# Kernel optimization log

Hardware: AMD Instinct MI355X
Metric: run time of the kernel (lower is better)

The kernel has to match this reference:

```python
import jax, jax.numpy as jnp
import numpy as np

EPS = 1e-6
ROPE_BASE = 10000.0


def rmsnorm(x, w):
    return x * jax.lax.rsqrt(jnp.mean(x * x, axis=-1, keepdims=True) + EPS) * w


def apply_rope(x, start_pos):
    # x: [B, H, S, Dh]
    B, H, S, Dh = x.shape
    inv_freq = 1.0 / (ROPE_BASE ** (jnp.arange(0, Dh, 2, dtype=jnp.float32) / Dh))
    pos = jnp.arange(S, dtype=jnp.float32) + start_pos
    ang = pos[:, None] * inv_freq[None, :]            # [S, Dh/2]
    cos, sin = jnp.cos(ang), jnp.sin(ang)
    x1, x2 = jnp.split(x, 2, axis=-1)
    return jnp.concatenate([x1 * cos - x2 * sin, x1 * sin + x2 * cos], axis=-1)


def block_forward(x, norm1_w, norm2_w, wq, w_dkv, w_uk, w_uv, wo, gate_w, w1, w2, w3, start_pos, n_head, d_head, top_k):
    B, S, D = x.shape
    E = w1.shape[0]

    # ---- MLA attention (pre-norm) ----
    h = rmsnorm(x, norm1_w)
    q = (h @ wq).reshape(B, S, n_head, d_head).transpose(0, 2, 1, 3)   # [B,H,S,Dh]
    c = h @ w_dkv                                                      # [B,S,d_latent]
    k = (c @ w_uk).reshape(B, S, n_head, d_head).transpose(0, 2, 1, 3)
    v = (c @ w_uv).reshape(B, S, n_head, d_head).transpose(0, 2, 1, 3)
    q = apply_rope(q, start_pos)
    k = apply_rope(k, start_pos)
    scores = jnp.einsum('bhqd,bhkd->bhqk', q, k) / jnp.sqrt(jnp.float32(d_head))
    causal = jnp.tril(jnp.ones((S, S), dtype=bool))
    scores = jnp.where(causal, scores, jnp.finfo(scores.dtype).min)
    attn = jax.nn.softmax(scores, axis=-1)
    a = jnp.einsum('bhqk,bhkd->bhqd', attn, v).transpose(0, 2, 1, 3).reshape(B, S, n_head * d_head)
    x = x + a @ wo

    # ---- MoE FFN (pre-norm) ----
    h2 = rmsnorm(x, norm2_w)
    xf = h2.reshape(B * S, D)                                          # [T,D]
    logits = xf @ gate_w                                               # [T,E]
    probs = jax.nn.softmax(logits, axis=-1)
    topv, topi = jax.lax.top_k(probs, top_k)                           # [T,k]
    topv = topv / jnp.sum(topv, axis=-1, keepdims=True)
    one_hot = jax.nn.one_hot(topi, E, dtype=probs.dtype)               # [T,k,E]
    combine = jnp.einsum('tk,tke->te', topv, one_hot)                  # [T,E]

    y = jnp.zeros_like(xf)
    for e in range(E):  # fixed small expert count; masked dense combine (no token drop)
        g = jax.nn.silu(xf @ w1[e]) * (xf @ w3[e])
        y = y + combine[:, e:e + 1] * (g @ w2[e])

    # load-balancing aux loss: E * sum(frac_routed * mean_prob)
    f = jnp.mean(one_hot, axis=(0, 1)) * top_k
    P = jnp.mean(probs, axis=0)
    aux_loss = jnp.float32(E) * jnp.sum(f * P)

    x = x + y.reshape(B, S, D)
    return x, aux_loss


def setup_inputs() -> dict:
    key = jax.random.key(0)
    D, H, Dh, DL, E, HID = 768, 12, 64, 64, 8, 4 * 768
    B, S = 2, 512
    ks = jax.random.split(key, 12)
    s = 0.02
    return {
        'x': jax.random.normal(ks[0], (B, S, D), jnp.float32),
        'norm1_w': jnp.ones((D,), jnp.float32),
        'norm2_w': jnp.ones((D,), jnp.float32),
        'wq': jax.random.normal(ks[1], (D, H * Dh), jnp.float32) * s,
        'w_dkv': jax.random.normal(ks[2], (D, DL), jnp.float32) * s,
        'w_uk': jax.random.normal(ks[3], (DL, H * Dh), jnp.float32) * s,
        'w_uv': jax.random.normal(ks[4], (DL, H * Dh), jnp.float32) * s,
        'wo': jax.random.normal(ks[5], (H * Dh, D), jnp.float32) * s,
        'gate_w': jax.random.normal(ks[6], (D, E), jnp.float32) * s,
        'w1': jax.random.normal(ks[7], (E, D, HID), jnp.float32) * s,
        'w2': jax.random.normal(ks[8], (E, HID, D), jnp.float32) * s,
        'w3': jax.random.normal(ks[9], (E, D, HID), jnp.float32) * s,
        'start_pos': 0,
    }


def reference(x, norm1_w, norm2_w, wq, w_dkv, w_uk, w_uv, wo, gate_w, w1, w2, w3, start_pos):
    return block_forward(x, norm1_w, norm2_w, wq, w_dkv, w_uk, w_uv, wo, gate_w, w1, w2, w3,
                         start_pos, n_head=12, d_head=64, top_k=2)
```

## Files before the change

kernel.cpp:

```cpp
#include <hip/hip_runtime.h>
#include <hip/hip_bf16.h>
#include <math.h>

#define T 1024
#define SEQ 512
#define BATCH 2
#define D 768
#define H 12
#define DH 64
#define DL 64
#define E 8
#define HID 3072

typedef __attribute__((ext_vector_type(8))) short bf16x8;
typedef __attribute__((ext_vector_type(4))) float f32x4;

__device__ inline short f2bf(float f) {
    __hip_bfloat16 h = __float2bfloat16(f);
    return *reinterpret_cast<short*>(&h);
}

__device__ inline void lds_barrier() {
    __builtin_amdgcn_sched_barrier(0);
    asm volatile("s_waitcnt lgkmcnt(0)" ::: "memory");
    __builtin_amdgcn_s_barrier();
    __builtin_amdgcn_sched_barrier(0);
}

__device__ inline int swz(int row, int k) { return (row * 64 + k) ^ ((row & 7) << 3); }
__device__ inline int swzB(int row, int k) { return row * 64 + (k ^ (((row >> 1) & 7) << 3)); }

__global__ void rmsnorm_kernel(const float* __restrict__ x, const float* __restrict__ w,
                               float* __restrict__ out, short* __restrict__ outb) {
    int t = blockIdx.x;
    int tid = threadIdx.x;
    const float* xr = x + (size_t)t * D;
    float s = 0.f;
    for (int i = tid; i < D; i += 256) { float v = xr[i]; s += v * v; }
    __shared__ float red[256];
    red[tid] = s; __syncthreads();
    for (int o = 128; o > 0; o >>= 1) { if (tid < o) red[tid] += red[tid + o]; __syncthreads(); }
    float scale = 1.0f / sqrtf(red[0] / (float)D + 1e-6f);
    for (int i = tid; i < D; i += 256) {
        float v = xr[i] * scale * w[i];
        out[(size_t)t * D + i] = v;
        outb[(size_t)t * D + i] = f2bf(v);
    }
}

template<bool RES>
__global__ __launch_bounds__(256) void gemm_bf16(
    const float* __restrict__ A, const float* __restrict__ B,
    const float* __restrict__ Rp, float* __restrict__ C,
    int M, int N, int K) {
    int mb = blockIdx.y * 64, nb = blockIdx.x * 64;
    __shared__ short As[64 * 64];
    __shared__ short Bs[64 * 64];
    int tid = threadIdx.x;
    int lane = tid & 63, wave = tid >> 6;
    int wr = wave >> 1, wc = wave & 1;
    f32x4 acc[2][2] = {};
    int ar = tid >> 2, ac = (tid & 3) * 16;
    int bn = (tid & 15) * 4, bk = (tid >> 4) * 4;
    const float* Arow = A + (size_t)(mb + ar) * K + ac;
    const float* Bg = B + nb;
    float4 a_r[4], b_r[4];
#pragma unroll
    for (int j = 0; j < 4; j++) a_r[j] = *(const float4*)(Arow + j * 4);
#pragma unroll
    for (int i = 0; i < 4; i++) b_r[i] = *(const float4*)(Bg + (size_t)(bk + i) * N + bn);
    for (int k0 = 0; k0 < K; k0 += 64) {
#pragma unroll
        for (int j = 0; j < 4; j++)
            *(short4*)&As[swzB(ar, ac + j * 4)] =
                make_short4(f2bf(a_r[j].x), f2bf(a_r[j].y), f2bf(a_r[j].z), f2bf(a_r[j].w));
        *(short4*)&Bs[swzB(bn + 0, bk)] = make_short4(f2bf(b_r[0].x), f2bf(b_r[1].x), f2bf(b_r[2].x), f2bf(b_r[3].x));
        *(short4*)&Bs[swzB(bn + 1, bk)] = make_short4(f2bf(b_r[0].y), f2bf(b_r[1].y), f2bf(b_r[2].y), f2bf(b_r[3].y));
        *(short4*)&Bs[swzB(bn + 2, bk)] = make_short4(f2bf(b_r[0].z), f2bf(b_r[1].z), f2bf(b_r[2].z), f2bf(b_r[3].z));
        *(short4*)&Bs[swzB(bn + 3, bk)] = make_short4(f2bf(b_r[0].w), f2bf(b_r[1].w), f2bf(b_r[2].w), f2bf(b_r[3].w));
        __syncthreads();
        bool more = (k0 + 64) < K;
        if (more) {
#pragma unroll
            for (int j = 0; j < 4; j++) a_r[j] = *(const float4*)(Arow + k0 + 64 + j * 4);
#pragma unroll
            for (int i = 0; i < 4; i++) b_r[i] = *(const float4*)(Bg + (size_t)(k0 + 64 + bk + i) * N + bn);
        }
#pragma unroll
        for (int kk = 0; kk < 64; kk += 32) {
            int krd = kk + 8 * (lane >> 4);
            bf16x8 a0 = *(const bf16x8*)&As[swzB(wr * 32 + (lane & 15), krd)];
            bf16x8 a1 = *(const bf16x8*)&As[swzB(wr * 32 + 16 + (lane & 15), krd)];
            bf16x8 b0 = *(const bf16x8*)&Bs[swzB(wc * 32 + (lane & 15), krd)];
            bf16x8 b1 = *(const bf16x8*)&Bs[swzB(wc * 32 + 16 + (lane & 15), krd)];
            acc[0][0] = __builtin_amdgcn_mfma_f32_16x16x32_bf16(a0, b0, acc[0][0], 0, 0, 0);
            acc[0][1] = __builtin_amdgcn_mfma_f32_16x16x32_bf16(a0, b1, acc[0][1], 0, 0, 0);
            acc[1][0] = __builtin_amdgcn_mfma_f32_16x16x32_bf16(a1, b0, acc[1][0], 0, 0, 0);
            acc[1][1] = __builtin_amdgcn_mfma_f32_16x16x32_bf16(a1, b1, acc[1][1], 0, 0, 0);
        }
        __syncthreads();
    }
#pragma unroll
    for (int mi = 0; mi < 2; mi++)
#pragma unroll
        for (int ni = 0; ni < 2; ni++)
#pragma unroll
            for (int r = 0; r < 4; r++) {
                int row = mb + wr * 32 + mi * 16 + (lane >> 4) * 4 + r;
                int col = nb + wc * 32 + ni * 16 + (lane & 15);
                float val = acc[mi][ni][r];
                if (RES) val += Rp[(size_t)row * N + col];
                C[(size_t)row * N + col] = val;
            }
}

__global__ __launch_bounds__(256) void gemm_qdkv(
    const float* __restrict__ A, const float* __restrict__ Bq, const float* __restrict__ Bd,
    float* __restrict__ Cq, float* __restrict__ Cd) {
    int bx = blockIdx.x;
    const float* Bsel; float* Csel; int N; int nb;
    if (bx < D / 64) { Bsel = Bq; Csel = Cq; N = D;  nb = bx * 64; }
    else             { Bsel = Bd; Csel = Cd; N = DL; nb = 0; }
    int mb = blockIdx.y * 64;
    __shared__ short As[64 * 64];
    __shared__ short Bs[64 * 64];
    int tid = threadIdx.x;
    int lane = tid & 63, wave = tid >> 6;
    int wr = wave >> 1, wc = wave & 1;
    f32x4 acc[2][2] = {};
    int ar = tid >> 2, ac = (tid & 3) * 16;
    int bn = (tid & 15) * 4, bk = (tid >> 4) * 4;
    const float* Arow = A + (size_t)(mb + ar) * D + ac;
    const float* Bg = Bsel + nb;
    float4 a_r[4], b_r[4];
#pragma unroll
    for (int j = 0; j < 4; j++) a_r[j] = *(const float4*)(Arow + j * 4);
#pragma unroll
    for (int i = 0; i < 4; i++) b_r[i] = *(const float4*)(Bg + (size_t)(bk + i) * N + bn);
    for (int k0 = 0; k0 < D; k0 += 64) {
#pragma unroll
        for (int j = 0; j < 4; j++)
            *(short4*)&As[swzB(ar, ac + j * 4)] =
                make_short4(f2bf(a_r[j].x), f2bf(a_r[j].y), f2bf(a_r[j].z), f2bf(a_r[j].w));
        *(short4*)&Bs[swzB(bn + 0, bk)] = make_short4(f2bf(b_r[0].x), f2bf(b_r[1].x), f2bf(b_r[2].x), f2bf(b_r[3].x));
        *(short4*)&Bs[swzB(bn + 1, bk)] = make_short4(f2bf(b_r[0].y), f2bf(b_r[1].y), f2bf(b_r[2].y), f2bf(b_r[3].y));
        *(short4*)&Bs[swzB(bn + 2, bk)] = make_short4(f2bf(b_r[0].z), f2bf(b_r[1].z), f2bf(b_r[2].z), f2bf(b_r[3].z));
        *(short4*)&Bs[swzB(bn + 3, bk)] = make_short4(f2bf(b_r[0].w), f2bf(b_r[1].w), f2bf(b_r[2].w), f2bf(b_r[3].w));
        __syncthreads();
        bool more = (k0 + 64) < D;
        if (more) {
#pragma unroll
            for (int j = 0; j < 4; j++) a_r[j] = *(const float4*)(Arow + k0 + 64 + j * 4);
#pragma unroll
            for (int i = 0; i < 4; i++) b_r[i] = *(const float4*)(Bg + (size_t)(k0 + 64 + bk + i) * N + bn);
        }
#pragma unroll
        for (int kk = 0; kk < 64; kk += 32) {
            int krd = kk + 8 * (lane >> 4);
            bf16x8 a0 = *(const bf16x8*)&As[swzB(wr * 32 + (lane & 15), krd)];
            bf16x8 a1 = *(const bf16x8*)&As[swzB(wr * 32 + 16 + (lane & 15), krd)];
            bf16x8 b0 = *(const bf16x8*)&Bs[swzB(wc * 32 + (lane & 15), krd)];
            bf16x8 b1 = *(const bf16x8*)&Bs[swzB(wc * 32 + 16 + (lane & 15), krd)];
            acc[0][0] = __builtin_amdgcn_mfma_f32_16x16x32_bf16(a0, b0, acc[0][0], 0, 0, 0);
            acc[0][1] = __builtin_amdgcn_mfma_f32_16x16x32_bf16(a0, b1, acc[0][1], 0, 0, 0);
            acc[1][0] = __builtin_amdgcn_mfma_f32_16x16x32_bf16(a1, b0, acc[1][0], 0, 0, 0);
            acc[1][1] = __builtin_amdgcn_mfma_f32_16x16x32_bf16(a1, b1, acc[1][1], 0, 0, 0);
        }
        __syncthreads();
    }
#pragma unroll
    for (int mi = 0; mi < 2; mi++)
#pragma unroll
        for (int ni = 0; ni < 2; ni++)
#pragma unroll
            for (int r = 0; r < 4; r++) {
                int row = mb + wr * 32 + mi * 16 + (lane >> 4) * 4 + r;
                int col = nb + wc * 32 + ni * 16 + (lane & 15);
                Csel[(size_t)row * N + col] = acc[mi][ni][r];
            }
}

__global__ __launch_bounds__(256) void gemm_kuv(
    const float* __restrict__ A, const float* __restrict__ Bk, const float* __restrict__ Bv,
    float* __restrict__ Ck, float* __restrict__ Cv, int M, int N, int K) {
    int mb = blockIdx.y * 64, nb = blockIdx.x * 64;
    __shared__ short As[64 * 64];
    __shared__ short B1s[64 * 64];
    __shared__ short B2s[64 * 64];
    int tid = threadIdx.x;
    int lane = tid & 63, wave = tid >> 6;
    int wr = wave >> 1, wc = wave & 1;
    f32x4 acc1[2][2] = {};
    f32x4 acc2[2][2] = {};
    int ar = tid >> 2, ac = (tid & 3) * 16;
    int bn = (tid & 15) * 4, bk = (tid >> 4) * 4;
    const float* Arow = A + (size_t)(mb + ar) * K + ac;
    {
        float4 a_c[4], p_c[4], q_c[4];
#pragma unroll
        for (int j = 0; j < 4; j++) a_c[j] = *(const float4*)(Arow + j * 4);
#pragma unroll
        for (int i = 0; i < 4; i++) {
            p_c[i] = *(const float4*)(Bk + (size_t)(bk + i) * N + nb + bn);
            q_c[i] = *(const float4*)(Bv + (size_t)(bk + i) * N + nb + bn);
        }
#pragma unroll
        for (int j = 0; j < 4; j++)
            *(short4*)&As[swzB(ar, ac + j * 4)] =
                make_short4(f2bf(a_c[j].x), f2bf(a_c[j].y), f2bf(a_c[j].z), f2bf(a_c[j].w));
        *(short4*)&B1s[swzB(bn + 0, bk)] = make_short4(f2bf(p_c[0].x), f2bf(p_c[1].x), f2bf(p_c[2].x), f2bf(p_c[3].x));
        *(short4*)&B1s[swzB(bn + 1, bk)] = make_short4(f2bf(p_c[0].y), f2bf(p_c[1].y), f2bf(p_c[2].y), f2bf(p_c[3].y));
        *(short4*)&B1s[swzB(bn + 2, bk)] = make_short4(f2bf(p_c[0].z), f2bf(p_c[1].z), f2bf(p_c[2].z), f2bf(p_c[3].z));
        *(short4*)&B1s[swzB(bn + 3, bk)] = make_short4(f2bf(p_c[0].w), f2bf(p_c[1].w), f2bf(p_c[2].w), f2bf(p_c[3].w));
        *(short4*)&B2s[swzB(bn + 0, bk)] = make_short4(f2bf(q_c[0].x), f2bf(q_c[1].x), f2bf(q_c[2].x), f2bf(q_c[3].x));
        *(short4*)&B2s[swzB(bn + 1, bk)] = make_short4(f2bf(q_c[0].y), f2bf(q_c[1].y), f2bf(q_c[2].y), f2bf(q_c[3].y));
        *(short4*)&B2s[swzB(bn + 2, bk)] = make_short4(f2bf(q_c[0].z), f2bf(q_c[1].z), f2bf(q_c[2].z), f2bf(q_c[3].z));
        *(short4*)&B2s[swzB(bn + 3, bk)] = make_short4(f2bf(q_c[0].w), f2bf(q_c[1].w), f2bf(q_c[2].w), f2bf(q_c[3].w));
    }
    __syncthreads();
#pragma unroll
    for (int kk = 0; kk < 64; kk += 32) {
        int krd = kk + 8 * (lane >> 4);
        bf16x8 a0 = *(const bf16x8*)&As[swzB(wr * 32 + (lane & 15), krd)];
        bf16x8 a1 = *(const bf16x8*)&As[swzB(wr * 32 + 16 + (lane & 15), krd)];
        bf16x8 p0 = *(const bf16x8*)&B1s[swzB(wc * 32 + (lane & 15), krd)];
        bf16x8 p1 = *(const bf16x8*)&B1s[swzB(wc * 32 + 16 + (lane & 15), krd)];
        bf16x8 q0 = *(const bf16x8*)&B2s[swzB(wc * 32 + (lane & 15), krd)];
        bf16x8 q1 = *(const bf16x8*)&B2s[swzB(wc * 32 + 16 + (lane & 15), krd)];
        acc1[0][0] = __builtin_amdgcn_mfma_f32_16x16x32_bf16(a0, p0, acc1[0][0], 0, 0, 0);
        acc1[0][1] = __builtin_amdgcn_mfma_f32_16x16x32_bf16(a0, p1, acc1[0][1], 0, 0, 0);
        acc1[1][0] = __builtin_amdgcn_mfma_f32_16x16x32_bf16(a1, p0, acc1[1][0], 0, 0, 0);
        acc1[1][1] = __builtin_amdgcn_mfma_f32_16x16x32_bf16(a1, p1, acc1[1][1], 0, 0, 0);
        acc2[0][0] = __builtin_amdgcn_mfma_f32_16x16x32_bf16(a0, q0, acc2[0][0], 0, 0, 0);
        acc2[0][1] = __builtin_amdgcn_mfma_f32_16x16x32_bf16(a0, q1, acc2[0][1], 0, 0, 0);
        acc2[1][0] = __builtin_amdgcn_mfma_f32_16x16x32_bf16(a1, q0, acc2[1][0], 0, 0, 0);
        acc2[1][1] = __builtin_amdgcn_mfma_f32_16x16x32_bf16(a1, q1, acc2[1][1], 0, 0, 0);
    }
#pragma unroll
    for (int mi = 0; mi < 2; mi++)
#pragma unroll
        for (int ni = 0; ni < 2; ni++)
#pragma unroll
            for (int r = 0; r < 4; r++) {
                int row = mb + wr * 32 + mi * 16 + (lane >> 4) * 4 + r;
                int col = nb + wc * 32 + ni * 16 + (lane & 15);
                Ck[(size_t)row * N + col] = acc1[mi][ni][r];
                Cv[(size_t)row * N + col] = acc2[mi][ni][r];
            }
}

__global__ void rope_kernel(float* __restrict__ qb, float* __restrict__ kb,
                            const int* __restrict__ spp) {
    int p = blockIdx.x * 256 + threadIdx.x;
    if (p >= T * H * 32) return;
    int i = p & 31;
    int rem = p >> 5;
    int h = rem % H;
    int ts = rem / H;
    int s = ts % SEQ;
    float invf = powf(10000.0f, -(float)(2 * i) / 64.0f);
    float ang = (float)(s + spp[0]) * invf;
    float c = cosf(ang), sn = sinf(ang);
    size_t base = (size_t)ts * D + h * DH;
    float x1 = qb[base + i], x2 = qb[base + 32 + i];
    qb[base + i] = x1 * c - x2 * sn;
    qb[base + 32 + i] = x1 * sn + x2 * c;
    x1 = kb[base + i]; x2 = kb[base + 32 + i];
    kb[base + i] = x1 * c - x2 * sn;
    kb[base + 32 + i] = x1 * sn + x2 * c;
}

__global__ __launch_bounds__(256) void attn_mfma(
    const float* __restrict__ q, const float* __restrict__ k,
    const float* __restrict__ v, float* __restrict__ a) {
    int qt = blockIdx.x, h = blockIdx.y, b = blockIdx.z;
    int tid = threadIdx.x, lane = tid & 63, wave = tid >> 6;
    __shared__ short Qs[64 * 64];
    __shared__ short Ks[64 * 64];
    __shared__ short Vs[64 * 64];
    __shared__ short Ps[64 * 64];
    int qbase = qt * 64;
    {
        int r = tid >> 2, d0 = (tid & 3) * 16;
        const float* src = q + ((size_t)(b * SEQ + qbase + r)) * D + h * DH + d0;
#pragma unroll
        for (int j = 0; j < 4; j++) {
            float4 vv = *(const float4*)(src + j * 4);
            *(short4*)&Qs[swz(r, d0 + j * 4)] =
                make_short4(f2bf(vv.x), f2bf(vv.y), f2bf(vv.z), f2bf(vv.w));
        }
    }
    __syncthreads();
    bf16x8 qf0 = *(const bf16x8*)&Qs[swz(wave * 16 + (lane & 15), 8 * (lane >> 4))];
    bf16x8 qf1 = *(const bf16x8*)&Qs[swz(wave * 16 + (lane & 15), 32 + 8 * (lane >> 4))];

    float m_run[4] = {-1e30f, -1e30f, -1e30f, -1e30f};
    float l_run[4] = {0.f, 0.f, 0.f, 0.f};
    f32x4 o[4] = {};

    for (int kt = 0; kt <= qt; kt++) {
        int kvbase = kt * 64;
        {
            int r = tid >> 2, d0 = (tid & 3) * 16;
            const float* src = k + ((size_t)(b * SEQ + kvbase + r)) * D + h * DH + d0;
#pragma unroll
            for (int j = 0; j < 4; j++) {
                float4 vv = *(const float4*)(src + j * 4);
                *(short4*)&Ks[swz(r, d0 + j * 4)] =
                    make_short4(f2bf(vv.x), f2bf(vv.y), f2bf(vv.z), f2bf(vv.w));
            }
        }
#pragma unroll
        for (int i = 0; i < 4; i++) {
            int idx = tid + i * 256;
            int kr = idx >> 4, d0 = (idx & 15) * 4;
            float4 vv = *(const float4*)(v + ((size_t)(b * SEQ + kvbase + kr)) * D + h * DH + d0);
            Vs[swz(d0 + 0, kr)] = f2bf(vv.x); Vs[swz(d0 + 1, kr)] = f2bf(vv.y);
            Vs[swz(d0 + 2, kr)] = f2bf(vv.z); Vs[swz(d0 + 3, kr)] = f2bf(vv.w);
        }
        __syncthreads();

        f32x4 s[4];
#pragma unroll
        for (int kvt = 0; kvt < 4; kvt++) {
            bf16x8 kf0 = *(const bf16x8*)&Ks[swz(kvt * 16 + (lane & 15), 8 * (lane >> 4))];
            bf16x8 kf1 = *(const bf16x8*)&Ks[swz(kvt * 16 + (lane & 15), 32 + 8 * (lane >> 4))];
            f32x4 z = {};
            z = __builtin_amdgcn_mfma_f32_16x16x32_bf16(qf0, kf0, z, 0, 0, 0);
            z = __builtin_amdgcn_mfma_f32_16x16x32_bf16(qf1, kf1, z, 0, 0, 0);
            s[kvt] = z;
        }
#pragma unroll
        for (int kvt = 0; kvt < 4; kvt++) {
#pragma unroll
            for (int r = 0; r < 4; r++) {
                float val = s[kvt][r] * 0.125f;
                if (kt == qt) {
                    int kv_abs = kvbase + kvt * 16 + (lane & 15);
                    int q_abs = qbase + wave * 16 + (lane >> 4) * 4 + r;
                    if (kv_abs > q_abs) val = -1e30f;
                }
                s[kvt][r] = val;
            }
        }
        float mnew[4], psum[4], scl[4];
#pragma unroll
        for (int r = 0; r < 4; r++) {
            float mx = fmaxf(fmaxf(s[0][r], s[1][r]), fmaxf(s[2][r], s[3][r]));
#pragma unroll
            for (int o2 = 8; o2 > 0; o2 >>= 1) mx = fmaxf(mx, __shfl_xor(mx, o2));
            mnew[r] = fmaxf(m_run[r], mx);
            float ps = 0.f;
#pragma unroll
            for (int kvt = 0; kvt < 4; kvt++) {
                float p = expf(s[kvt][r] - mnew[r]);
                s[kvt][r] = p;
                ps += p;
            }
#pragma unroll
            for (int o2 = 8; o2 > 0; o2 >>= 1) ps += __shfl_xor(ps, o2);
            psum[r] = ps;
            scl[r] = expf(m_run[r] - mnew[r]);
            m_run[r] = mnew[r];
            l_run[r] = l_run[r] * scl[r] + psum[r];
        }
#pragma unroll
        for (int dt = 0; dt < 4; dt++)
#pragma unroll
            for (int r = 0; r < 4; r++) o[dt][r] *= scl[r];
#pragma unroll
        for (int kvt = 0; kvt < 4; kvt++)
#pragma unroll
            for (int r = 0; r < 4; r++)
                Ps[swz(wave * 16 + (lane >> 4) * 4 + r, kvt * 16 + (lane & 15))] = f2bf(s[kvt][r]);
        __syncthreads();
        bf16x8 pa0 = *(const bf16x8*)&Ps[swz(wave * 16 + (lane & 15), 8 * (lane >> 4))];
        bf16x8 pa1 = *(const bf16x8*)&Ps[swz(wave * 16 + (lane & 15), 32 + 8 * (lane >> 4))];
#pragma unroll
        for (int dt = 0; dt < 4; dt++) {
            bf16x8 vf0 = *(const bf16x8*)&Vs[swz(dt * 16 + (lane & 15), 8 * (lane >> 4))];
            bf16x8 vf1 = *(const bf16x8*)&Vs[swz(dt * 16 + (lane & 15), 32 + 8 * (lane >> 4))];
            o[dt] = __builtin_amdgcn_mfma_f32_16x16x32_bf16(pa0, vf0, o[dt], 0, 0, 0);
            o[dt] = __builtin_amdgcn_mfma_f32_16x16x32_bf16(pa1, vf1, o[dt], 0, 0, 0);
        }
        __syncthreads();
    }
#pragma unroll
    for (int r = 0; r < 4; r++) {
        float inv = 1.0f / l_run[r];
        int qrow = qbase + wave * 16 + (lane >> 4) * 4 + r;
#pragma unroll
        for (int dt = 0; dt < 4; dt++) {
            a[((size_t)(b * SEQ + qrow)) * D + h * DH + dt * 16 + (lane & 15)] = o[dt][r] * inv;
        }
    }
}

__global__ void routing_kernel(const float* __restrict__ h2, const float* __restrict__ gw,
                               float* __restrict__ probs, int* __restrict__ list,
                               int* __restrict__ counts, float* __restrict__ wtok) {
    int t = blockIdx.x;
    int tid = threadIdx.x;
    __shared__ float part[64][8];
    float l[8] = {0.f, 0.f, 0.f, 0.f, 0.f, 0.f, 0.f, 0.f};
    const float* hr = h2 + (size_t)t * D;
    for (int i = tid; i < D; i += 64) {
        float hv = hr[i];
        const float* g = gw + (size_t)i * E;
#pragma unroll
        for (int e = 0; e < 8; e++) l[e] += hv * g[e];
    }
#pragma unroll
    for (int e = 0; e < 8; e++) part[tid][e] = l[e];
    __syncthreads();
    if (tid == 0) {
        float lg[8];
#pragma unroll
        for (int e = 0; e < 8; e++) {
            float s = 0.f;
            for (int j = 0; j < 64; j++) s += part[j][e];
            lg[e] = s;
        }
        float m = lg[0];
#pragma unroll
        for (int e = 1; e < 8; e++) m = fmaxf(m, lg[e]);
        float se = 0.f;
        float pr[8];
#pragma unroll
        for (int e = 0; e < 8; e++) { pr[e] = expf(lg[e] - m); se += pr[e]; }
#pragma unroll
        for (int e = 0; e < 8; e++) { pr[e] /= se; probs[t * 8 + e] = pr[e]; }
        int i0 = 0;
#pragma unroll
        for (int e = 1; e < 8; e++) if (pr[e] > pr[i0]) i0 = e;
        int i1 = -1;
#pragma unroll
        for (int e = 0; e < 8; e++) {
            if (e == i0) continue;
            if (i1 < 0 || pr[e] > pr[i1]) i1 = e;
        }
        float w0 = pr[i0], w1 = pr[i1];
        float wsum = w0 + w1;
        wtok[t * 2 + 0] = w0 / wsum;
        wtok[t * 2 + 1] = w1 / wsum;
        int p0 = atomicAdd(&counts[i0], 1); list[i0 * T + p0] = t * 2 + 0;
        int p1 = atomicAdd(&counts[i1], 1); list[i1 * T + p1] = t * 2 + 1;
    }
}

__global__ void moe_setup_kernel(const int* __restrict__ counts,
                                 int* __restrict__ m2e_u, int* __restrict__ m2mb_u,
                                 int* __restrict__ m2e_d, int* __restrict__ m2mb_d,
                                 int* __restrict__ ntm) {
    if (threadIdx.x == 0 && blockIdx.x == 0) {
        int idx = 0;
        for (int e = 0; e < E; e++) {
            int nt = (counts[e] + 127) >> 7;
            for (int i = 0; i < nt; i++) { m2e_u[idx] = e; m2mb_u[idx] = i * 128; idx++; }
        }
        ntm[0] = idx;
        idx = 0;
        for (int e = 0; e < E; e++) {
            int nt = (counts[e] + 63) >> 6;
            for (int i = 0; i < nt; i++) { m2e_d[idx] = e; m2mb_d[idx] = i * 64; idx++; }
        }
        ntm[1] = idx;
    }
}

__global__ void aux_kernel(const float* __restrict__ probs, const int* __restrict__ counts,
                           float* __restrict__ out_aux) {
    int tid = threadIdx.x;
    float part[8] = {0.f, 0.f, 0.f, 0.f, 0.f, 0.f, 0.f, 0.f};
    for (int t = tid; t < T; t += 256) {
#pragma unroll
        for (int e = 0; e < 8; e++) part[e] += probs[t * 8 + e];
    }
    __shared__ float red[256][8];
#pragma unroll
    for (int e = 0; e < 8; e++) red[tid][e] = part[e];
    __syncthreads();
    for (int o = 128; o > 0; o >>= 1) {
        if (tid < o) {
#pragma unroll
            for (int e = 0; e < 8; e++) red[tid][e] += red[tid + o][e];
        }
        __syncthreads();
    }
    if (tid == 0) {
        float aux = 0.f;
        for (int e = 0; e < 8; e++) {
            float f = (float)counts[e] / (float)T;
            float P = red[0][e] / (float)T;
            aux += f * P;
        }
        out_aux[0] = (float)E * aux;
    }
}

__global__ __launch_bounds__(256) void moe_up_mfma(
    const short* __restrict__ h2b, const float* __restrict__ w1, const float* __restrict__ w3,
    const int* __restrict__ list, const int* __restrict__ counts,
    const int* __restrict__ m2e, const int* __restrict__ m2mb, const int* __restrict__ ntm,
    short* __restrict__ g) {
    int mi = blockIdx.y;
    if (mi >= ntm[0]) return;
    int e = m2e[mi];
    int mb = m2mb[mi];
    int n = counts[e];
    int nb = blockIdx.x * 64;
    const float* B1g = w1 + (size_t)e * D * HID + nb;
    const float* B3g = w3 + (size_t)e * D * HID + nb;
    __shared__ short As[2][128 * 64];
    __shared__ short B1s[2][64 * 64];
    __shared__ short B3s[2][64 * 64];
    __shared__ int rowpid[128];
    __shared__ int rowtok[128];
    int tid = threadIdx.x;
    int lane = tid & 63, wave = tid >> 6;
    int wr = wave >> 1, wc = wave & 1;
    if (tid < 128) {
        int r = mb + tid;
        int pid = (r < n) ? list[e * T + r] : list[e * T];
        rowpid[tid] = pid;
        rowtok[tid] = pid >> 1;
    }
    __syncthreads();

    f32x4 acc1[4][2] = {};
    f32x4 acc3[4][2] = {};
    int ar = tid >> 1, ac = (tid & 1) * 32;
    int bn = (tid & 15) * 4, bk = (tid >> 4) * 4;
    const short* Arow = h2b + (size_t)rowtok[ar] * D + ac;

    bf16x8 a_r[4];
    float4 b1_r[4], b3_r[4];
#pragma unroll
    for (int j = 0; j < 4; j++) a_r[j] = *(const bf16x8*)(Arow + j * 8);
#pragma unroll
    for (int i = 0; i < 4; i++) {
        b1_r[i] = *(const float4*)(B1g + (size_t)(bk + i) * HID + bn);
        b3_r[i] = *(const float4*)(B3g + (size_t)(bk + i) * HID + bn);
    }
#pragma unroll
    for (int j = 0; j < 4; j++) *(bf16x8*)&As[0][swzB(ar, ac + j * 8)] = a_r[j];
    *(short4*)&B1s[0][swzB(bn + 0, bk)] = make_short4(f2bf(b1_r[0].x), f2bf(b1_r[1].x), f2bf(b1_r[2].x), f2bf(b1_r[3].x));
    *(short4*)&B1s[0][swzB(bn + 1, bk)] = make_short4(f2bf(b1_r[0].y), f2bf(b1_r[1].y), f2bf(b1_r[2].y), f2bf(b1_r[3].y));
    *(short4*)&B1s[0][swzB(bn + 2, bk)] = make_short4(f2bf(b1_r[0].z), f2bf(b1_r[1].z), f2bf(b1_r[2].z), f2bf(b1_r[3].z));
    *(short4*)&B1s[0][swzB(bn + 3, bk)] = make_short4(f2bf(b1_r[0].w), f2bf(b1_r[1].w), f2bf(b1_r[2].w), f2bf(b1_r[3].w));
    *(short4*)&B3s[0][swzB(bn + 0, bk)] = make_short4(f2bf(b3_r[0].x), f2bf(b3_r[1].x), f2bf(b3_r[2].x), f2bf(b3_r[3].x));
    *(short4*)&B3s[0][swzB(bn + 1, bk)] = make_short4(f2bf(b3_r[0].y), f2bf(b3_r[1].y), f2bf(b3_r[2].y), f2bf(b3_r[3].y));
    *(short4*)&B3s[0][swzB(bn + 2, bk)] = make_short4(f2bf(b3_r[0].z), f2bf(b3_r[1].z), f2bf(b3_r[2].z), f2bf(b3_r[3].z));
    *(short4*)&B3s[0][swzB(bn + 3, bk)] = make_short4(f2bf(b3_r[0].w), f2bf(b3_r[1].w), f2bf(b3_r[2].w), f2bf(b3_r[3].w));
    lds_barrier();
#pragma unroll
    for (int j = 0; j < 4; j++) a_r[j] = *(const bf16x8*)(Arow + 64 + j * 8);
#pragma unroll
    for (int i = 0; i < 4; i++) {
        b1_r[i] = *(const float4*)(B1g + (size_t)(64 + bk + i) * HID + bn);
        b3_r[i] = *(const float4*)(B3g + (size_t)(64 + bk + i) * HID + bn);
    }

    int cur = 0;
    for (int k0 = 0; k0 < D; k0 += 64) {
        bool more = (k0 + 64) < D;
        if (more) {
            int nx = cur ^ 1;
#pragma unroll
            for (int j = 0; j < 4; j++) *(bf16x8*)&As[nx][swzB(ar, ac + j * 8)] = a_r[j];
            *(short4*)&B1s[nx][swzB(bn + 0, bk)] = make_short4(f2bf(b1_r[0].x), f2bf(b1_r[1].x), f2bf(b1_r[2].x), f2bf(b1_r[3].x));
            *(short4*)&B1s[nx][swzB(bn + 1, bk)] = make_short4(f2bf(b1_r[0].y), f2bf(b1_r[1].y), f2bf(b1_r[2].y), f2bf(b1_r[3].y));
            *(short4*)&B1s[nx][swzB(bn + 2, bk)] = make_short4(f2bf(b1_r[0].z), f2bf(b1_r[1].z), f2bf(b1_r[2].z), f2bf(b1_r[3].z));
            *(short4*)&B1s[nx][swzB(bn + 3, bk)] = make_short4(f2bf(b1_r[0].w), f2bf(b1_r[1].w), f2bf(b1_r[2].w), f2bf(b1_r[3].w));
            *(short4*)&B3s[nx][swzB(bn + 0, bk)] = make_short4(f2bf(b3_r[0].x), f2bf(b3_r[1].x), f2bf(b3_r[2].x), f2bf(b3_r[3].x));
            *(short4*)&B3s[nx][swzB(bn + 1, bk)] = make_short4(f2bf(b3_r[0].y), f2bf(b3_r[1].y), f2bf(b3_r[2].y), f2bf(b3_r[3].y));
            *(short4*)&B3s[nx][swzB(bn + 2, bk)] = make_short4(f2bf(b3_r[0].z), f2bf(b3_r[1].z), f2bf(b3_r[2].z), f2bf(b3_r[3].z));
            *(short4*)&B3s[nx][swzB(bn + 3, bk)] = make_short4(f2bf(b3_r[0].w), f2bf(b3_r[1].w), f2bf(b3_r[2].w), f2bf(b3_r[3].w));
        }
        if (k0 + 128 < D) {
#pragma unroll
            for (int j = 0; j < 4; j++) a_r[j] = *(const bf16x8*)(Arow + k0 + 128 + j * 8);
#pragma unroll
            for (int i = 0; i < 4; i++) {
                b1_r[i] = *(const float4*)(B1g + (size_t)(k0 + 128 + bk + i) * HID + bn);
                b3_r[i] = *(const float4*)(B3g + (size_t)(k0 + 128 + bk + i) * HID + bn);
            }
        }
#pragma unroll
        for (int kk = 0; kk < 64; kk += 32) {
            int krd = kk + 8 * (lane >> 4);
            bf16x8 b1f[2], b3f[2];
#pragma unroll
            for (int ni = 0; ni < 2; ni++) {
                b1f[ni] = *(const bf16x8*)&B1s[cur][swzB(wc * 32 + ni * 16 + (lane & 15), krd)];
                b3f[ni] = *(const bf16x8*)&B3s[cur][swzB(wc * 32 + ni * 16 + (lane & 15), krd)];
            }
#pragma unroll
            for (int mi2 = 0; mi2 < 4; mi2++) {
                bf16x8 af = *(const bf16x8*)&As[cur][swzB(wr * 64 + mi2 * 16 + (lane & 15), krd)];
                acc1[mi2][0] = __builtin_amdgcn_mfma_f32_16x16x32_bf16(af, b1f[0], acc1[mi2][0], 0, 0, 0);
                acc1[mi2][1] = __builtin_amdgcn_mfma_f32_16x16x32_bf16(af, b1f[1], acc1[mi2][1], 0, 0, 0);
                acc3[mi2][0] = __builtin_amdgcn_mfma_f32_16x16x32_bf16(af, b3f[0], acc3[mi2][0], 0, 0, 0);
                acc3[mi2][1] = __builtin_amdgcn_mfma_f32_16x16x32_bf16(af, b3f[1], acc3[mi2][1], 0, 0, 0);
            }
        }
        lds_barrier();
        cur ^= 1;
    }
#pragma unroll
    for (int mi2 = 0; mi2 < 4; mi2++)
#pragma unroll
        for (int ni = 0; ni < 2; ni++)
#pragma unroll
            for (int r = 0; r < 4; r++) {
                int row = wr * 64 + mi2 * 16 + (lane >> 4) * 4 + r;
                if (mb + row < n) {
                    int pid = rowpid[row];
                    int col = nb + wc * 32 + ni * 16 + (lane & 15);
                    float v1 = acc1[mi2][ni][r], v3 = acc3[mi2][ni][r];
                    float sil = v1 / (1.f + expf(-v1));
                    g[(size_t)pid * HID + col] = f2bf(sil * v3);
                }
            }
}

__global__ __launch_bounds__(256) void moe_down_mfma(
    const short* __restrict__ g, const float* __restrict__ w2,
    const int* __restrict__ list, const int* __restrict__ counts,
    const int* __restrict__ m2e, const int* __restrict__ m2mb, const int* __restrict__ ntm,
    float* __restrict__ yp) {
    int mi = blockIdx.y;
    if (mi >= ntm[1]) return;
    int e = m2e[mi];
    int mb = m2mb[mi];
    int n = counts[e];
    int nb = blockIdx.x * 64;
    const float* Bg = w2 + (size_t)e * HID * D + nb;
    __shared__ short As[64 * 64];
    __shared__ short Bs[64 * 64];
    __shared__ int rowpid[64];
    int tid = threadIdx.x;
    int lane = tid & 63, wave = tid >> 6;
    int wr = wave >> 1, wc = wave & 1;
    if (tid < 64) {
        int r = mb + tid;
        rowpid[tid] = (r < n) ? list[e * T + r] : list[e * T];
    }
    __syncthreads();

    f32x4 acc[2][2] = {};
    int ar0 = tid >> 3, ak0 = (tid & 7) * 8;
    int ar1 = (tid + 256) >> 3, ak1 = ((tid + 256) & 7) * 8;
    int bn = (tid & 15) * 4, bk = (tid >> 4) * 4;
    const short* Asrc0 = g + (size_t)rowpid[ar0] * HID + ak0;
    const short* Asrc1 = g + (size_t)rowpid[ar1] * HID + ak1;

    bf16x8 a_r0 = *(const bf16x8*)(Asrc0);
    bf16x8 a_r1 = *(const bf16x8*)(Asrc1);
    float4 b_r[4];
#pragma unroll
    for (int i = 0; i < 4; i++) b_r[i] = *(const float4*)(Bg + (size_t)(bk + i) * D + bn);

    for (int k0 = 0; k0 < HID; k0 += 64) {
        *(bf16x8*)&As[swzB(ar0, ak0)] = a_r0;
        *(bf16x8*)&As[swzB(ar1, ak1)] = a_r1;
        *(short4*)&Bs[swzB(bn + 0, bk)] = make_short4(f2bf(b_r[0].x), f2bf(b_r[1].x), f2bf(b_r[2].x), f2bf(b_r[3].x));
        *(short4*)&Bs[swzB(bn + 1, bk)] = make_short4(f2bf(b_r[0].y), f2bf(b_r[1].y), f2bf(b_r[2].y), f2bf(b_r[3].y));
        *(short4*)&Bs[swzB(bn + 2, bk)] = make_short4(f2bf(b_r[0].z), f2bf(b_r[1].z), f2bf(b_r[2].z), f2bf(b_r[3].z));
        *(short4*)&Bs[swzB(bn + 3, bk)] = make_short4(f2bf(b_r[0].w), f2bf(b_r[1].w), f2bf(b_r[2].w), f2bf(b_r[3].w));
        lds_barrier();
        bool more = (k0 + 64) < HID;
        if (more) {
            a_r0 = *(const bf16x8*)(Asrc0 + k0 + 64);
            a_r1 = *(const bf16x8*)(Asrc1 + k0 + 64);
#pragma unroll
            for (int i = 0; i < 4; i++) b_r[i] = *(const float4*)(Bg + (size_t)(k0 + 64 + bk + i) * D + bn);
        }
#pragma unroll
        for (int kk = 0; kk < 64; kk += 32) {
            int krd = kk + 8 * (lane >> 4);
            bf16x8 a0 = *(const bf16x8*)&As[swzB(wr * 32 + (lane & 15), krd)];
            bf16x8 a1 = *(const bf16x8*)&As[swzB(wr * 32 + 16 + (lane & 15), krd)];
            bf16x8 b0 = *(const bf16x8*)&Bs[swzB(wc * 32 + (lane & 15), krd)];
            bf16x8 b1 = *(const bf16x8*)&Bs[swzB(wc * 32 + 16 + (lane & 15), krd)];
            acc[0][0] = __builtin_amdgcn_mfma_f32_16x16x32_bf16(a0, b0, acc[0][0], 0, 0, 0);
            acc[0][1] = __builtin_amdgcn_mfma_f32_16x16x32_bf16(a0, b1, acc[0][1], 0, 0, 0);
            acc[1][0] = __builtin_amdgcn_mfma_f32_16x16x32_bf16(a1, b0, acc[1][0], 0, 0, 0);
            acc[1][1] = __builtin_amdgcn_mfma_f32_16x16x32_bf16(a1, b1, acc[1][1], 0, 0, 0);
        }
        lds_barrier();
    }
#pragma unroll
    for (int mi2 = 0; mi2 < 2; mi2++)
#pragma unroll
        for (int ni = 0; ni < 2; ni++)
#pragma unroll
            for (int r = 0; r < 4; r++) {
                int row = wr * 32 + mi2 * 16 + (lane >> 4) * 4 + r;
                if (mb + row < n) {
                    int pid = rowpid[row];
                    int col = nb + wc * 32 + ni * 16 + (lane & 15);
                    yp[(size_t)pid * D + col] = acc[mi2][ni][r];
                }
            }
}

__global__ void combine_kernel(const float* __restrict__ yp, const float* __restrict__ wtok,
                               float* __restrict__ out) {
    int idx = blockIdx.x * 256 + threadIdx.x;
    if (idx >= T * (D / 4)) return;
    int t = idx / (D / 4);
    int d4 = idx % (D / 4);
    float4 a = ((const float4*)(out + (size_t)t * D))[d4];
    float4 y0 = ((const float4*)(yp + (size_t)(2 * t) * D))[d4];
    float4 y1 = ((const float4*)(yp + (size_t)(2 * t + 1) * D))[d4];
    float w0 = wtok[2 * t], w1 = wtok[2 * t + 1];
    a.x += w0 * y0.x + w1 * y1.x;
    a.y += w0 * y0.y + w1 * y1.y;
    a.z += w0 * y0.z + w1 * y1.z;
    a.w += w0 * y0.w + w1 * y1.w;
    ((float4*)(out + (size_t)t * D))[d4] = a;
}

extern "C" void kernel_launch(void* const* d_in, const int* in_sizes, int n_in,
                              void* d_out, int out_size, void* d_ws, size_t ws_size,
                              hipStream_t stream) {
    const float* x    = (const float*)d_in[0];
    const float* n1w  = (const float*)d_in[1];
    const float* n2w  = (const float*)d_in[2];
    const float* wq   = (const float*)d_in[3];
    const float* wdkv = (const float*)d_in[4];
    const float* wuk  = (const float*)d_in[5];
    const float* wuv  = (const float*)d_in[6];
    const float* wo   = (const float*)d_in[7];
    const float* gw   = (const float*)d_in[8];
    const float* w1   = (const float*)d_in[9];
    const float* w2   = (const float*)d_in[10];
    const float* w3   = (const float*)d_in[11];
    const int*   sp   = (const int*)d_in[12];
    float* out = (float*)d_out;

    float* ws = (float*)d_ws;
    float* A_  = ws + 0;
    float* B_  = ws + 786432;
    float* C_  = ws + 1572864;
    float* Dd  = ws + 2359296;
    float* cb  = ws + 3145728;
    float* probs = ws + 3211264;
    float* wtok  = ws + 3219456;
    int*   list  = (int*)(ws + 3221504);
    int*   counts= (int*)(ws + 3229696);
    int*   m2e_u = (int*)(ws + 3229712);
    int*   m2mb_u= (int*)(ws + 3229744);
    int*   m2e_d = (int*)(ws + 3229776);
    int*   m2mb_d= (int*)(ws + 3229840);
    int*   ntm   = (int*)(ws + 3229904);
    short* h2b   = (short*)(ws + 3229920);
    short* gch   = (short*)(ws + 3623136);
    float* yp = B_;

    hipMemsetAsync(counts, 0, 16 * sizeof(int), stream);

    rmsnorm_kernel<<<T, 256, 0, stream>>>(x, n1w, Dd, h2b);
    gemm_qdkv<<<dim3(D / 64 + 1, T / 64), 256, 0, stream>>>(Dd, wq, wdkv, A_, cb);
    gemm_kuv<<<dim3(D / 64, T / 64), 256, 0, stream>>>(cb, wuk, wuv, B_, C_, T, D, DL);
    rope_kernel<<<(T * H * 32 + 255) / 256, 256, 0, stream>>>(A_, B_, sp);
    attn_mfma<<<dim3(8, H, BATCH), 256, 0, stream>>>(A_, B_, C_, Dd);
    gemm_bf16<true><<<dim3(D / 64, T / 64), 256, 0, stream>>>(Dd, wo, x, out, T, D, D);

    rmsnorm_kernel<<<T, 256, 0, stream>>>(out, n2w, A_, h2b);
    routing_kernel<<<T, 64, 0, stream>>>(A_, gw, probs, list, counts, wtok);
    moe_setup_kernel<<<1, 64, 0, stream>>>(counts, m2e_u, m2mb_u, m2e_d, m2mb_d, ntm);
    aux_kernel<<<1, 256, 0, stream>>>(probs, counts, out + (out_size - 1));
    moe_up_mfma<<<dim3(HID / 64, 32), 256, 0, stream>>>(h2b, w1, w3, list, counts, m2e_u, m2mb_u, ntm, gch);
    moe_down_mfma<<<dim3(D / 64, 40), 256, 0, stream>>>(gch, w2, list, counts, m2e_d, m2mb_d, ntm, yp);
    combine_kernel<<<(T * (D / 4) + 255) / 256, 256, 0, stream>>>(yp, wtok, out);
}
```

Baseline: 219.9 us.

## Enlarge MoE down-proj M tile to 128 and double-buffer LDS

The MoE down-projection kernel now processes 128 token rows per block instead of 64, reusing the up-projection's 128-row tile mapping (m2e_u/m2mb_u, ntm[0]). It also double-buffers the A and B LDS tiles, so each iteration needs only one barrier and the global loads run two steps ahead. The larger tile halves the number of w2 tile reads and raises MFMA work per B fragment. In exchange LDS use and register pressure grow, and fewer blocks are launched, which can lower occupancy.

```diff
diff --git a/kernel.cpp b/kernel.cpp
--- a/kernel.cpp
+++ b/kernel.cpp
@@ -630,73 +630,89 @@
     const int* __restrict__ m2e, const int* __restrict__ m2mb, const int* __restrict__ ntm,
     float* __restrict__ yp) {
     int mi = blockIdx.y;
-    if (mi >= ntm[1]) return;
+    if (mi >= ntm[0]) return;
     int e = m2e[mi];
     int mb = m2mb[mi];
     int n = counts[e];
     int nb = blockIdx.x * 64;
     const float* Bg = w2 + (size_t)e * HID * D + nb;
-    __shared__ short As[64 * 64];
-    __shared__ short Bs[64 * 64];
-    __shared__ int rowpid[64];
+    __shared__ short As[2][128 * 64];
+    __shared__ short Bs[2][64 * 64];
+    __shared__ int rowpid[128];
     int tid = threadIdx.x;
     int lane = tid & 63, wave = tid >> 6;
     int wr = wave >> 1, wc = wave & 1;
-    if (tid < 64) {
+    if (tid < 128) {
         int r = mb + tid;
         rowpid[tid] = (r < n) ? list[e * T + r] : list[e * T];
     }
     __syncthreads();
 
-    f32x4 acc[2][2] = {};
-    int ar0 = tid >> 3, ak0 = (tid & 7) * 8;
-    int ar1 = (tid + 256) >> 3, ak1 = ((tid + 256) & 7) * 8;
+    f32x4 acc[4][2] = {};
+    int ar = tid >> 1, ac = (tid & 1) * 32;
     int bn = (tid & 15) * 4, bk = (tid >> 4) * 4;
-    const short* Asrc0 = g + (size_t)rowpid[ar0] * HID + ak0;
-    const short* Asrc1 = g + (size_t)rowpid[ar1] * HID + ak1;
-
-    bf16x8 a_r0 = *(const bf16x8*)(Asrc0);
-    bf16x8 a_r1 = *(const bf16x8*)(Asrc1);
+    const short* Arow = g + (size_t)rowpid[ar] * HID + ac;
+
+    bf16x8 a_r[4];
     float4 b_r[4];
 #pragma unroll
+    for (int j = 0; j < 4; j++) a_r[j] = *(const bf16x8*)(Arow + j * 8);
+#pragma unroll
     for (int i = 0; i < 4; i++) b_r[i] = *(const float4*)(Bg + (size_t)(bk + i) * D + bn);
-
+#pragma unroll
+    for (int j = 0; j < 4; j++) *(bf16x8*)&As[0][swzB(ar, ac + j * 8)] = a_r[j];
+    *(short4*)&Bs[0][swzB(bn + 0, bk)] = make_short4(f2bf(b_r[0].x), f2bf(b_r[1].x), f2bf(b_r[2].x), f2bf(b_r[3].x));
+    *(short4*)&Bs[0][swzB(bn + 1, bk)] = make_short4(f2bf(b_r[0].y), f2bf(b_r[1].y), f2bf(b_r[2].y), f2bf(b_r[3].y));
+    *(short4*)&Bs[0][swzB(bn + 2, bk)] = make_short4(f2bf(b_r[0].z), f2bf(b_r[1].z), f2bf(b_r[2].z), f2bf(b_r[3].z));
+    *(short4*)&Bs[0][swzB(bn + 3, bk)] = make_short4(f2bf(b_r[0].w), f2bf(b_r[1].w), f2bf(b_r[2].w), f2bf(b_r[3].w));
+    lds_barrier();
+#pragma unroll
+    for (int j = 0; j < 4; j++) a_r[j] = *(const bf16x8*)(Arow + 64 + j * 8);
+#pragma unroll
+    for (int i = 0; i < 4; i++) b_r[i] = *(const float4*)(Bg + (size_t)(64 + bk + i) * D + bn);
+
+    int cur = 0;
     for (int k0 = 0; k0 < HID; k0 += 64) {
-        *(bf16x8*)&As[swzB(ar0, ak0)] = a_r0;
-        *(bf16x8*)&As[swzB(ar1, ak1)] = a_r1;
-        *(short4*)&Bs[swzB(bn + 0, bk)] = make_short4(f2bf(b_r[0].x), f2bf(b_r[1].x), f2bf(b_r[2].x), f2bf(b_r[3].x));
-        *(short4*)&Bs[swzB(bn + 1, bk)] = make_short4(f2bf(b_r[0].y), f2bf(b_r[1].y), f2bf(b_r[2].y), f2bf(b_r[3].y));
-        *(short4*)&Bs[swzB(bn + 2, bk)] = make_short4(f2bf(b_r[0].z), f2bf(b_r[1].z), f2bf(b_r[2].z), f2bf(b_r[3].z));
-        *(short4*)&Bs[swzB(bn + 3, bk)] = make_short4(f2bf(b_r[0].w), f2bf(b_r[1].w), f2bf(b_r[2].w), f2bf(b_r[3].w));
-        lds_barrier();
         bool more = (k0 + 64) < HID;
         if (more) {
-            a_r0 = *(const bf16x8*)(Asrc0 + k0 + 64);
-            a_r1 = *(const bf16x8*)(Asrc1 + k0 + 64);
-#pragma unroll
-            for (int i = 0; i < 4; i++) b_r[i] = *(const float4*)(Bg + (size_t)(k0 + 64 + bk + i) * D + bn);
+            int nx = cur ^ 1;
+#pragma unroll
+            for (int j = 0; j < 4; j++) *(bf16x8*)&As[nx][swzB(ar, ac + j * 8)] = a_r[j];
+            *(short4*)&Bs[nx][swzB(bn + 0, bk)] = make_short4(f2bf(b_r[0].x), f2bf(b_r[1].x), f2bf(b_r[2].x), f2bf(b_r[3].x));
+            *(short4*)&Bs[nx][swzB(bn + 1, bk)] = make_short4(f2bf(b_r[0].y), f2bf(b_r[1].y), f2bf(b_r[2].y), f2bf(b_r[3].y));
+            *(short4*)&Bs[nx][swzB(bn + 2, bk)] = make_short4(f2bf(b_r[0].z), f2bf(b_r[1].z), f2bf(b_r[2].z), f2bf(b_r[3].z));
+            *(short4*)&Bs[nx][swzB(bn + 3, bk)] = make_short4(f2bf(b_r[0].w), f2bf(b_r[1].w), f2bf(b_r[2].w), f2bf(b_r[3].w));
+        }
+        if (k0 + 128 < HID) {
+#pragma unroll
+            for (int j = 0; j < 4; j++) a_r[j] = *(const bf16x8*)(Arow + k0 + 128 + j * 8);
+#pragma unroll
+            for (int i = 0; i < 4; i++) b_r[i] = *(const float4*)(Bg + (size_t)(k0 + 128 + bk + i) * D + bn);
         }
 #pragma unroll
         for (int kk = 0; kk < 64; kk += 32) {
             int krd = kk + 8 * (lane >> 4);
-            bf16x8 a0 = *(const bf16x8*)&As[swzB(wr * 32 + (lane & 15), krd)];
-            bf16x8 a1 = *(const bf16x8*)&As[swzB(wr * 32 + 16 + (lane & 15), krd)];
-            bf16x8 b0 = *(const bf16x8*)&Bs[swzB(wc * 32 + (lane & 15), krd)];
-            bf16x8 b1 = *(const bf16x8*)&Bs[swzB(wc * 32 + 16 + (lane & 15), krd)];
-            acc[0][0] = __builtin_amdgcn_mfma_f32_16x16x32_bf16(a0, b0, acc[0][0], 0, 0, 0);
-            acc[0][1] = __builtin_amdgcn_mfma_f32_16x16x32_bf16(a0, b1, acc[0][1], 0, 0, 0);
-            acc[1][0] = __builtin_amdgcn_mfma_f32_16x16x32_bf16(a1, b0, acc[1][0], 0, 0, 0);
-            acc[1][1] = __builtin_amdgcn_mfma_f32_16x16x32_bf16(a1, b1, acc[1][1], 0, 0, 0);
+            bf16x8 bf[2];
+#pragma unroll
+            for (int ni = 0; ni < 2; ni++)
+                bf[ni] = *(const bf16x8*)&Bs[cur][swzB(wc * 32 + ni * 16 + (lane & 15), krd)];
+#pragma unroll
+            for (int mi2 = 0; mi2 < 4; mi2++) {
+                bf16x8 af = *(const bf16x8*)&As[cur][swzB(wr * 64 + mi2 * 16 + (lane & 15), krd)];
+                acc[mi2][0] = __builtin_amdgcn_mfma_f32_16x16x32_bf16(af, bf[0], acc[mi2][0], 0, 0, 0);
+                acc[mi2][1] = __builtin_amdgcn_mfma_f32_16x16x32_bf16(af, bf[1], acc[mi2][1], 0, 0, 0);
+            }
         }
         lds_barrier();
-    }
-#pragma unroll
-    for (int mi2 = 0; mi2 < 2; mi2++)
+        cur ^= 1;
+    }
+#pragma unroll
+    for (int mi2 = 0; mi2 < 4; mi2++)
 #pragma unroll
         for (int ni = 0; ni < 2; ni++)
 #pragma unroll
             for (int r = 0; r < 4; r++) {
-                int row = wr * 32 + mi2 * 16 + (lane >> 4) * 4 + r;
+                int row = wr * 64 + mi2 * 16 + (lane >> 4) * 4 + r;
                 if (mb + row < n) {
                     int pid = rowpid[row];
                     int col = nb + wc * 32 + ni * 16 + (lane & 15);
@@ -773,6 +789,6 @@
     moe_setup_kernel<<<1, 64, 0, stream>>>(counts, m2e_u, m2mb_u, m2e_d, m2mb_d, ntm);
     aux_kernel<<<1, 256, 0, stream>>>(probs, counts, out + (out_size - 1));
     moe_up_mfma<<<dim3(HID / 64, 32), 256, 0, stream>>>(h2b, w1, w3, list, counts, m2e_u, m2mb_u, ntm, gch);
-    moe_down_mfma<<<dim3(D / 64, 40), 256, 0, stream>>>(gch, w2, list, counts, m2e_d, m2mb_d, ntm, yp);
+    moe_down_mfma<<<dim3(D / 64, 32), 256, 0, stream>>>(gch, w2, list, counts, m2e_u, m2mb_u, ntm, yp);
     combine_kernel<<<(T * (D / 4) + 255) / 256, 256, 0, stream>>>(yp, wtok, out);
 }
```

Result: no change. 220.7 us (+0.4%).
